# Performance work log

Hardware: AMD Instinct MI355X
Metric: run time of the kernel (lower is better)

Reference implementation:

```python
import jax, jax.numpy as jnp
import numpy as np

HEADS = 8
TQ, QH, QW = 4, 16, 16
TK, KH, KW = 4, 16, 16
DIM = 64


def setup_inputs() -> dict:
    key = jax.random.key(0)
    k1, k2, k3, k4, k5 = jax.random.split(key, 5)
    return {
        "query": jax.random.normal(k1, (4, HEADS, TQ * QH * QW, DIM), dtype=jnp.float32),
        "scores": jax.random.normal(k2, (4, HEADS, TQ * QH * QW, TK * KH * KW), dtype=jnp.float32),
        "height_embeddings": jax.random.normal(k3, (2 * (max(QH, KH) - 1) + 1, DIM), dtype=jnp.float32),
        "width_embeddings": jax.random.normal(k4, (2 * (max(QW, KW) - 1) + 1, DIM), dtype=jnp.float32),
        "time_embeddings": jax.random.normal(k5, (2 * (max(TQ, TK) - 1) + 1, DIM), dtype=jnp.float32),
    }


def _rel_dist(q_n, k_n):
    # matches torch: ratios are both 1 when q_n == k_n
    q_ratio = round(max(k_n / q_n, 1.0))
    k_ratio = round(max(q_n / k_n, 1.0))
    d = jnp.arange(q_n)[:, None] * q_ratio - jnp.arange(k_n)[None, :] * k_ratio
    return d + (k_n - 1) * k_ratio  # [q_n, k_n] int indices


def reference(query, scores, height_embeddings, width_embeddings, time_embeddings):
    Rh = height_embeddings[_rel_dist(QH, KH)]  # [QH, KH, DIM]
    Rw = width_embeddings[_rel_dist(QW, KW)]   # [QW, KW, DIM]
    Rt = time_embeddings[_rel_dist(TQ, TK)]    # [TQ, TK, DIM]

    q = query.reshape(-1, HEADS, TQ, QH, QW, DIM)
    rel_h = jnp.einsum('bNthwc,hkc->bNthwk', q, Rh)  # [B,N,T,H,W,KH]
    rel_w = jnp.einsum('bNthwc,wkc->bNthwk', q, Rw)  # [B,N,T,H,W,KW]
    rel_t = jnp.einsum('bNthwc,tkc->bNthwk', q, Rt)  # [B,N,T,H,W,TK]

    s = scores.reshape(-1, HEADS, TQ, QH, QW, TK, KH, KW)
    s = (s
         + rel_h[:, :, :, :, :, None, :, None]
         + rel_w[:, :, :, :, :, None, None, :]
         + rel_t[:, :, :, :, :, :, None, None])
    return s.reshape(-1, HEADS, TQ * QH * QW, TK * KH * KW)
```

## Files before the change

kernel.cpp:

```cpp
#include <hip/hip_runtime.h>

#define NHEADS 8
#define TQ 4
#define QH 16
#define QW 16
#define TK 4
#define KH 16
#define KW 16
#define DIM 64
#define BATCH 4

#define ROWS (BATCH * NHEADS * TQ * QH * QW)
#define RPB 16
#define EST 68

typedef float f4 __attribute__((ext_vector_type(4)));

__global__ __launch_bounds__(256) void relpos_stage_kernel(
    const float* __restrict__ query,
    const float* __restrict__ scores,
    const float* __restrict__ hemb,
    const float* __restrict__ wemb,
    const float* __restrict__ temb,
    float* __restrict__ out)
{
    const int tid  = threadIdx.x;
    const int lane = tid & 63;
    const int wv   = tid >> 6;
    const int row0 = blockIdx.x * RPB;
    const int pos  = row0 & 1023;
    const int t = pos >> 8;
    const int h = (pos >> 4) & 15;

    __shared__ float lds_q[RPB][EST];
    __shared__ float lds_h[16][EST];
    __shared__ float lds_w[31][EST];
    __shared__ float lds_t[4][EST];
    __shared__ float rel[RPB][40];

    {
        const f4* sq = (const f4*)(query + (size_t)row0 * DIM);
        const f4* sh = (const f4*)(hemb + (size_t)h * DIM);
        const f4* sw = (const f4*)wemb;
        const f4* st = (const f4*)(temb + (size_t)t * DIM);
        {
            const int r = tid >> 4, c = tid & 15;
            *(f4*)&lds_q[r][4 * c] = sq[tid];
            *(f4*)&lds_h[r][4 * c] = sh[tid];
            *(f4*)&lds_w[r][4 * c] = sw[tid];
        }
        if (tid < 240) {
            const int k = 256 + tid;
            *(f4*)&lds_w[k >> 4][4 * (k & 15)] = sw[k];
        }
        if (tid < 64)
            *(f4*)&lds_t[tid >> 4][4 * (tid & 15)] = st[tid];
    }
    __syncthreads();

    const size_t rbase = (size_t)(row0 + wv * 4) * 1024;
    f4 s[4][4];
#pragma unroll
    for (int r = 0; r < 4; ++r) {
        const f4* sp = (const f4*)(scores + rbase + (size_t)r * 1024);
#pragma unroll
        for (int i = 0; i < 4; ++i)
            s[r][i] = __builtin_nontemporal_load(sp + lane + 64 * i);
    }

#pragma unroll
    for (int d0 = 0; d0 < 144; d0 += 64) {
        const int d = d0 + lane;
        if (d < 144) {
            const int rl  = d / 36;
            const int j   = d - rl * 36;
            const int row = wv * 4 + rl;
            const float* ep;
            if (j < 16)      ep = &lds_h[15 - j][0];
            else if (j < 32) ep = &lds_w[row - (j - 16) + 15][0];
            else             ep = &lds_t[3 - (j - 32)][0];
            const float* qp = &lds_q[row][0];
            float acc = 0.f;
#pragma unroll
            for (int c = 0; c < 16; ++c) {
                f4 qv = *(const f4*)(qp + 4 * c);
                f4 ev = *(const f4*)(ep + 4 * c);
                acc += qv.x * ev.x + qv.y * ev.y + qv.z * ev.z + qv.w * ev.w;
            }
            rel[row][j] = acc;
        }
    }

    const int kh  = lane >> 2;
    const int kw0 = (lane << 2) & 15;
#pragma unroll
    for (int r = 0; r < 4; ++r) {
        const int row = wv * 4 + r;
        const float hv = rel[row][kh];
        const f4 tv  = *(const f4*)&rel[row][32];
        const f4 wv4 = *(const f4*)&rel[row][16 + kw0];
        f4* op = (f4*)(out + rbase + (size_t)r * 1024);
#pragma unroll
        for (int i = 0; i < 4; ++i) {
            f4 o = s[r][i] + (hv + tv[i]) + wv4;
            __builtin_nontemporal_store(o, op + lane + 64 * i);
        }
    }
}

extern "C" void kernel_launch(void* const* d_in, const int* in_sizes, int n_in,
                              void* d_out, int out_size, void* d_ws, size_t ws_size,
                              hipStream_t stream) {
    const float* query  = (const float*)d_in[0];
    const float* scores = (const float*)d_in[1];
    const float* hemb   = (const float*)d_in[2];
    const float* wemb   = (const float*)d_in[3];
    const float* temb   = (const float*)d_in[4];
    float* out = (float*)d_out;

    relpos_stage_kernel<<<dim3(ROWS / RPB), dim3(256), 0, stream>>>(
        query, scores, hemb, wemb, temb, out);
}
```

Baseline: 236.6 us.

## Split bias computation into separate kernel and stream scores with double-buffered rows

Computes the per-row height+time and width bias vectors in a first kernel and writes them to workspace. A second streaming kernel then reads scores, adds the precomputed biases and writes the output, double-buffering two rows per wave so loads overlap stores. The goal is to take the dot-product compute and LDS staging off the bandwidth-bound streaming path. In exchange it adds a second launch and extra workspace traffic (about 20 MB written and read back). It falls back to the fused kernel when no workspace is available.

```diff
diff --git a/kernel.cpp b/kernel.cpp
--- a/kernel.cpp
+++ b/kernel.cpp
@@ -13,8 +13,134 @@
 #define ROWS (BATCH * NHEADS * TQ * QH * QW)
 #define RPB 16
 #define EST 68
+#define WS_BYTES_NEEDED ((size_t)ROWS * 80 * sizeof(float))
 
 typedef float f4 __attribute__((ext_vector_type(4)));
+
+__global__ __launch_bounds__(256) void relpos_bias16(
+    const float* __restrict__ query,
+    const float* __restrict__ hemb,
+    const float* __restrict__ wemb,
+    const float* __restrict__ temb,
+    float* __restrict__ thp,
+    float* __restrict__ wt)
+{
+    const int tid  = threadIdx.x;
+    const int lane = tid & 63;
+    const int wv   = tid >> 6;
+    const int row0 = blockIdx.x * RPB;
+    const int pos  = row0 & 1023;
+    const int t = pos >> 8;
+    const int h = (pos >> 4) & 15;
+
+    __shared__ float lds_q[RPB][EST];
+    __shared__ float lds_h[16][EST];
+    __shared__ float lds_w[31][EST];
+    __shared__ float lds_t[4][EST];
+    __shared__ float rel[RPB][40];
+
+    {
+        const f4* sq = (const f4*)(query + (size_t)row0 * DIM);
+        const f4* sh = (const f4*)(hemb + (size_t)h * DIM);
+        const f4* sw = (const f4*)wemb;
+        const f4* st = (const f4*)(temb + (size_t)t * DIM);
+        {
+            const int r = tid >> 4, c = tid & 15;
+            *(f4*)&lds_q[r][4 * c] = sq[tid];
+            *(f4*)&lds_h[r][4 * c] = sh[tid];
+            *(f4*)&lds_w[r][4 * c] = sw[tid];
+        }
+        if (tid < 240) {
+            const int k = 256 + tid;
+            *(f4*)&lds_w[k >> 4][4 * (k & 15)] = sw[k];
+        }
+        if (tid < 64)
+            *(f4*)&lds_t[tid >> 4][4 * (tid & 15)] = st[tid];
+    }
+    __syncthreads();
+
+#pragma unroll
+    for (int d0 = 0; d0 < 144; d0 += 64) {
+        const int d = d0 + lane;
+        if (d < 144) {
+            const int rl  = d / 36;
+            const int j   = d - rl * 36;
+            const int row = wv * 4 + rl;
+            const float* ep;
+            if (j < 16)      ep = &lds_h[15 - j][0];
+            else if (j < 32) ep = &lds_w[row - (j - 16) + 15][0];
+            else             ep = &lds_t[3 - (j - 32)][0];
+            const float* qp = &lds_q[row][0];
+            float acc = 0.f;
+#pragma unroll
+            for (int c = 0; c < 16; ++c) {
+                f4 qv = *(const f4*)(qp + 4 * c);
+                f4 ev = *(const f4*)(ep + 4 * c);
+                acc += qv.x * ev.x + qv.y * ev.y + qv.z * ev.z + qv.w * ev.w;
+            }
+            rel[row][j] = acc;
+        }
+    }
+
+    float* tb = thp + (size_t)(row0 + wv * 4) * 64;
+    float* wb = wt  + (size_t)(row0 + wv * 4) * 16;
+#pragma unroll
+    for (int r = 0; r < 4; ++r) {
+        const int lr = wv * 4 + r;
+        tb[r * 64 + lane] = rel[lr][lane >> 2] + rel[lr][32 + (lane & 3)];
+        if (lane < 16) wb[r * 16 + lane] = rel[lr][16 + lane];
+    }
+}
+
+__global__ __launch_bounds__(256) void relpos_stream_kernel(
+    const float* __restrict__ scores,
+    const float* __restrict__ thp,
+    const float* __restrict__ wt,
+    float* __restrict__ out)
+{
+    const int lane = threadIdx.x & 63;
+    const int wv   = threadIdx.x >> 6;
+    const size_t row0 = ((size_t)blockIdx.x * 4 + wv) * 8;
+
+    const f4* sp = (const f4*)scores + row0 * 256;
+    f4*       op = (f4*)out          + row0 * 256;
+    const int khq = lane >> 2;
+    const int wq  = lane & 3;
+
+    f4 sA0, sA1, sA2, sA3, thA, wA;
+    f4 sB0, sB1, sB2, sB3, thB, wB;
+
+#define LDROW(S0, S1, S2, S3, TH, W, r)                                        \
+    {                                                                          \
+        const f4* p = sp + (r) * 256;                                          \
+        S0 = __builtin_nontemporal_load(p + lane);                             \
+        S1 = __builtin_nontemporal_load(p + lane + 64);                        \
+        S2 = __builtin_nontemporal_load(p + lane + 128);                       \
+        S3 = __builtin_nontemporal_load(p + lane + 192);                       \
+        TH = *((const f4*)(thp + (row0 + (r)) * 64) + khq);                    \
+        W  = *((const f4*)(wt  + (row0 + (r)) * 16) + wq);                     \
+    }
+#define STROW(S0, S1, S2, S3, TH, W, r)                                        \
+    {                                                                          \
+        f4* p = op + (r) * 256;                                                \
+        __builtin_nontemporal_store(S0 + TH[0] + W, p + lane);                 \
+        __builtin_nontemporal_store(S1 + TH[1] + W, p + lane + 64);            \
+        __builtin_nontemporal_store(S2 + TH[2] + W, p + lane + 128);           \
+        __builtin_nontemporal_store(S3 + TH[3] + W, p + lane + 192);           \
+    }
+
+    LDROW(sA0, sA1, sA2, sA3, thA, wA, 0)
+#pragma unroll
+    for (int k = 0; k < 4; ++k) {
+        LDROW(sB0, sB1, sB2, sB3, thB, wB, 2 * k + 1)
+        STROW(sA0, sA1, sA2, sA3, thA, wA, 2 * k)
+        if (2 * k + 2 < 8)
+            LDROW(sA0, sA1, sA2, sA3, thA, wA, 2 * k + 2)
+        STROW(sB0, sB1, sB2, sB3, thB, wB, 2 * k + 1)
+    }
+#undef LDROW
+#undef STROW
+}
 
 __global__ __launch_bounds__(256) void relpos_stage_kernel(
     const float* __restrict__ query,
@@ -118,6 +244,15 @@
     const float* temb   = (const float*)d_in[4];
     float* out = (float*)d_out;
 
-    relpos_stage_kernel<<<dim3(ROWS / RPB), dim3(256), 0, stream>>>(
-        query, scores, hemb, wemb, temb, out);
-}
+    if (d_ws != nullptr && ws_size >= WS_BYTES_NEEDED) {
+        float* thp = (float*)d_ws;
+        float* wt  = thp + (size_t)ROWS * 64;
+        relpos_bias16<<<dim3(ROWS / RPB), dim3(256), 0, stream>>>(
+            query, hemb, wemb, temb, thp, wt);
+        relpos_stream_kernel<<<dim3(ROWS / 32), dim3(256), 0, stream>>>(
+            scores, thp, wt, out);
+    } else {
+        relpos_stage_kernel<<<dim3(ROWS / RPB), dim3(256), 0, stream>>>(
+            query, scores, hemb, wemb, temb, out);
+    }
+}
```

After: 245.2 us. 3.6% more time.
